# Kernel tuning notes

Measured on AMD Instinct MI355X. Metric: run time of the kernel, lower is better.

## Reference

```python
import jax, jax.numpy as jnp
import numpy as np
from jax import lax

B, T, D, K = 2, 4096, 128, 256


def setup_inputs() -> dict:
    key = jax.random.key(0)
    ks = jax.random.split(key, 5)
    s = 0.05
    return {
        "z": jax.random.normal(ks[0], (B, T, D), jnp.float32),
        "conv_kernel": jax.random.normal(ks[1], (K, 1, D), jnp.float32) * s,  # flax WIO depthwise
        "conv_bias": jnp.zeros((D,), jnp.float32),
        "Wq": jax.random.normal(ks[2], (D, D), jnp.float32) * s,
        "bq": jnp.zeros((D,), jnp.float32),
        "Wk": jax.random.normal(ks[3], (D, D), jnp.float32) * s,
        "bk": jnp.zeros((D,), jnp.float32),
        "Wo": jax.random.normal(ks[4], (D, D), jnp.float32) * s,
        "bo": jnp.zeros((D,), jnp.float32),
    }


def _sphere_norm(x):
    return x / jnp.maximum(jnp.linalg.norm(x, axis=-1, keepdims=True), 1e-8)


def reference(z, conv_kernel, conv_bias, Wq, bq, Wk, bk, Wo, bo):
    Bv, Tv, Dv = z.shape
    Kv = conv_kernel.shape[0]

    # Depthwise causal memory conv (flax nn.Conv, padding='CAUSAL', groups=D)
    memory_force = lax.conv_general_dilated(
        z, conv_kernel, window_strides=(1,), padding=[(Kv - 1, 0)],
        dimension_numbers=("NWC", "WIO", "NWC"), feature_group_count=Dv,
    ) + conv_bias

    # Keys are computed from the base point z once, shared across RK4 stages
    k_hat = _sphere_norm(z @ Wk + bk)  # [B,T,D]
    mask = jnp.tril(jnp.ones((Tv, Tv), z.dtype))  # causal mask

    def vector_field(z_curr):
        q_hat = _sphere_norm(z_curr @ Wq + bq)
        dots = jnp.einsum("btd,bsd->bts", q_hat, k_hat)  # [B,T,T]
        attn = jnp.sin(dots) * mask  # Kuramoto-style sin coupling, causal
        kuramoto = jnp.einsum("bts,bsd->btd", attn, k_hat) @ Wo + bo
        total = memory_force + kuramoto
        # project to tangent space of the sphere at z_curr
        return total - jnp.sum(total * z_curr, axis=-1, keepdims=True) * z_curr

    h = 1.0

    def retract(z_base, v):
        return _sphere_norm(z_base + v)

    k1 = vector_field(z)
    k2 = vector_field(retract(z, 0.5 * h * k1))
    k3 = vector_field(retract(z, 0.5 * h * k2))
    k4 = vector_field(retract(z, h * k3))
    v_final = (h / 6.0) * (k1 + 2 * k2 + 2 * k3 + k4)
    return retract(z, v_final)
```

## Files before the change

### kernel.cpp

```cpp
#include <hip/hip_runtime.h>
#include <hip/hip_bf16.h>

#define BB 2
#define TT 4096
#define DD 128
#define KK 256
#define NROW (BB*TT)
#define NELT (NROW*DD)

typedef _Float16 f16;
typedef __attribute__((ext_vector_type(8))) f16 half8;
typedef __attribute__((ext_vector_type(2))) __fp16 fp16x2;
typedef __attribute__((ext_vector_type(4))) float f32x4;
typedef __attribute__((ext_vector_type(2))) int i32x2;

__device__ __forceinline__ int pack2(float a, float b){
  fp16x2 h = __builtin_amdgcn_cvt_pkrtz(a, b);
  return __builtin_bit_cast(int, h);
}

__device__ __forceinline__ void stage_w_f16(int tid, const float* __restrict__ W, f16* Wh){
  #pragma unroll
  for (int it = 0; it < 8; it++){
    int idx = tid + it*256;
    f32x4 a = *(const f32x4*)(W + (size_t)idx*8);
    f32x4 b = *(const f32x4*)(W + (size_t)idx*8 + 4);
    half8 h;
    #pragma unroll
    for (int u = 0; u < 4; u++){ h[u] = (f16)a[u]; h[4+u] = (f16)b[u]; }
    *(half8*)(Wh + (size_t)idx*8) = h;
  }
}

__device__ __forceinline__ void proj_norm_rows(
    int tid, int r0,
    const float* __restrict__ src, const float* __restrict__ W, const float* __restrict__ bias,
    f16* __restrict__ dst, f16* __restrict__ dstT)
{
  __shared__ f16 Wh[DD*DD];
  __shared__ float zs[32*DD];
  stage_w_f16(tid, W, Wh);
  #pragma unroll
  for (int it = 0; it < 4; it++){
    int idx = tid + it*256;
    *(f32x4*)(zs + idx*4) = *(const f32x4*)(src + (size_t)r0*DD + idx*4);
  }
  __syncthreads();
  int c = tid & 15, rr = tid >> 4;
  float acc0[8], acc1[8];
  #pragma unroll
  for (int u = 0; u < 8; u++){ float bv = bias[c*8+u]; acc0[u] = bv; acc1[u] = bv; }
  const float* zr0 = zs + rr*DD;
  const float* zr1 = zs + (rr+16)*DD;
  #pragma unroll 4
  for (int i = 0; i < DD; i++){
    half8 wv = *(const half8*)(Wh + i*DD + c*8);
    float a0 = zr0[i], a1 = zr1[i];
    #pragma unroll
    for (int u = 0; u < 8; u++){
      float w = (float)wv[u];
      acc0[u] = fmaf(a0, w, acc0[u]);
      acc1[u] = fmaf(a1, w, acc1[u]);
    }
  }
  float s0 = 0.f, s1 = 0.f;
  #pragma unroll
  for (int u = 0; u < 8; u++){ s0 = fmaf(acc0[u], acc0[u], s0); s1 = fmaf(acc1[u], acc1[u], s1); }
  #pragma unroll
  for (int m = 1; m < 16; m <<= 1){ s0 += __shfl_xor(s0, m, 16); s1 += __shfl_xor(s1, m, 16); }
  float inv0 = 1.f / fmaxf(sqrtf(s0), 1e-8f);
  float inv1 = 1.f / fmaxf(sqrtf(s1), 1e-8f);
  half8 h0, h1;
  #pragma unroll
  for (int u = 0; u < 8; u++){ h0[u] = (f16)(acc0[u]*inv0); h1[u] = (f16)(acc1[u]*inv1); }
  int row0 = r0 + rr, row1 = row0 + 16;
  *(half8*)(dst + (size_t)row0*DD + c*8) = h0;
  *(half8*)(dst + (size_t)row1*DD + c*8) = h1;
  if (dstT){
    int b = row0 >> 12, t0 = row0 & 4095, t1 = row1 & 4095;
    #pragma unroll
    for (int u = 0; u < 8; u++){
      dstT[((size_t)b*DD + c*8 + u)*TT + t0] = h0[u];
      dstT[((size_t)b*DD + c*8 + u)*TT + t1] = h1[u];
    }
  }
}

__global__ __launch_bounds__(256) void k_prep(
    const float* __restrict__ z, const float* __restrict__ Wk, const float* __restrict__ bk,
    const float* __restrict__ ck, const float* __restrict__ cb,
    const float* __restrict__ Wq, const float* __restrict__ bq,
    f16* __restrict__ khb, f16* __restrict__ khT, f16* __restrict__ qhb,
    float* __restrict__ mf)
{
  int tid = threadIdx.x;
  if (blockIdx.x < 512){
    int bid = blockIdx.x;
    int d = tid & 127, tg = tid >> 7;
    int b = bid >> 8;
    int tbase = ((bid & 255) << 4) + tg*8;
    const float* zb = z + (size_t)b*TT*DD;
    float acc[8];
    #pragma unroll
    for (int j = 0; j < 8; j++) acc[j] = 0.f;
    float ckq[8];
    #pragma unroll
    for (int u = 0; u < 8; u++) ckq[u] = 0.f;
    int sstart = tbase - (KK-1);
    for (int ch = 0; ch < 33; ch++){
      #pragma unroll
      for (int u = 0; u < 8; u++){
        int base = ch*8 + u;
        int s = sstart + base;
        float zv = ((unsigned)s < (unsigned)TT && base < 263) ? zb[(size_t)s*DD + d] : 0.f;
        ckq[u] = (base < KK) ? ck[(size_t)base*DD + d] : 0.f;
        #pragma unroll
        for (int j = 0; j < 8; j++) acc[j] = fmaf(ckq[(u-j)&7], zv, acc[j]);
      }
    }
    float cbv = cb[d];
    #pragma unroll
    for (int j = 0; j < 8; j++)
      mf[((size_t)b*TT + tbase + j)*DD + d] = acc[j] + cbv;
  } else if (blockIdx.x < 768){
    proj_norm_rows(tid, (blockIdx.x - 512) * 32, z, Wk, bk, khb, khT);
  } else {
    proj_norm_rows(tid, (blockIdx.x - 768) * 32, z, Wq, bq, qhb, nullptr);
  }
}

#define QTILE 128
#define NQT3 (TT/QTILE)
#define NCHUNK 144

__global__ __launch_bounds__(256,2) void k_attn13(
    const f16* __restrict__ qhb, const f16* __restrict__ khb,
    const f16* __restrict__ khT, f16* __restrict__ part)
{
  int bid = blockIdx.x;
  int b = bid / NCHUNK;
  int rem = bid - b*NCHUNK;
  int qt = 0, chunk = 0;
  #pragma unroll 1
  for (int j = NQT3-1; j >= 0; j--){
    int nch = (j + 4) >> 2;
    if (rem < nch){ qt = j; chunk = rem; break; }
    rem -= nch;
  }
  int kt0 = chunk * 8;
  int kt1 = min(kt0 + 7, 2*qt + 1);
  int t0 = qt * QTILE;

  __shared__ __align__(16) f16 Kb[64*136];
  __shared__ __align__(16) f16 Kt[128*72];
  __shared__ __align__(16) f16 Ps[4][32*72];

  int tid  = threadIdx.x;
  int w    = tid >> 6;
  int lane = tid & 63;
  int n16  = lane & 15;
  int g    = lane >> 4;

  const f16* qg  = qhb + (size_t)b*TT*DD;
  const f16* kg  = khb + (size_t)b*TT*DD;
  const f16* ktg = khT + (size_t)b*DD*TT;

  int sb_r  = tid >> 4, sb_c = (tid & 15)*8;
  int st_r  = tid >> 3, st_c = (tid & 7)*8;

  half8 qa[2][4];
  #pragma unroll
  for (int p = 0; p < 2; p++){
    const f16* qrow = qg + (size_t)(t0 + 32*w + 16*p + n16)*DD + g*8;
    #pragma unroll
    for (int c = 0; c < 4; c++) qa[p][c] = *(const half8*)(qrow + 32*c);
  }
  f32x4 acc[2][8];
  #pragma unroll
  for (int p = 0; p < 2; p++)
    #pragma unroll
    for (int i = 0; i < 8; i++) acc[p][i] = (f32x4){0.f,0.f,0.f,0.f};

  f16* psw = &Ps[w][0];

  half8 sKb[4], sKt[4];
  {
    int s0 = kt0 * 64;
    #pragma unroll
    for (int it = 0; it < 4; it++)
      sKb[it] = *(const half8*)(kg + (size_t)(s0 + sb_r + it*16)*DD + sb_c);
    #pragma unroll
    for (int it = 0; it < 4; it++)
      sKt[it] = *(const half8*)(ktg + (size_t)(st_r + it*32)*TT + s0 + st_c);
  }

  for (int kt = kt0; kt <= kt1; kt++){
    #pragma unroll
    for (int it = 0; it < 4; it++)
      *(half8*)(Kb + (sb_r + it*16)*136 + sb_c) = sKb[it];
    #pragma unroll
    for (int it = 0; it < 4; it++)
      *(half8*)(Kt + (st_r + it*32)*72 + st_c) = sKt[it];
    __syncthreads();

    if (kt < kt1){
      int s0n = (kt+1) * 64;
      #pragma unroll
      for (int it = 0; it < 4; it++)
        sKb[it] = *(const half8*)(kg + (size_t)(s0n + sb_r + it*16)*DD + sb_c);
      #pragma unroll
      for (int it = 0; it < 4; it++)
        sKt[it] = *(const half8*)(ktg + (size_t)(st_r + it*32)*TT + s0n + st_c);
    }

    int s0 = kt * 64;
    f32x4 s_acc[2][4];
    #pragma unroll
    for (int p = 0; p < 2; p++)
      #pragma unroll
      for (int n = 0; n < 4; n++) s_acc[p][n] = (f32x4){0.f,0.f,0.f,0.f};
    #pragma unroll
    for (int c = 0; c < 4; c++){
      #pragma unroll
      for (int n = 0; n < 4; n++){
        half8 af = *(const half8*)(Kb + (16*n + n16)*136 + 32*c + g*8);
        s_acc[0][n] = __builtin_amdgcn_mfma_f32_16x16x32_f16(af, qa[0][c], s_acc[0][n], 0,0,0);
        s_acc[1][n] = __builtin_amdgcn_mfma_f32_16x16x32_f16(af, qa[1][c], s_acc[1][n], 0,0,0);
      }
    }
    #pragma unroll
    for (int p = 0; p < 2; p++){
      int qrow = t0 + 32*w + 16*p + n16;
      #pragma unroll
      for (int n = 0; n < 4; n++){
        int keyr = s0 + 16*n + 4*g;
        float v0 = (keyr     <= qrow) ? __sinf(s_acc[p][n][0]) : 0.f;
        float v1 = (keyr + 1 <= qrow) ? __sinf(s_acc[p][n][1]) : 0.f;
        float v2 = (keyr + 2 <= qrow) ? __sinf(s_acc[p][n][2]) : 0.f;
        float v3 = (keyr + 3 <= qrow) ? __sinf(s_acc[p][n][3]) : 0.f;
        i32x2 pw = { pack2(v0, v1), pack2(v2, v3) };
        *(i32x2*)(psw + (16*p + n16)*72 + 16*n + 4*g) = pw;
      }
    }

    #pragma unroll
    for (int h = 0; h < 2; h++){
      half8 pa[2];
      #pragma unroll
      for (int p = 0; p < 2; p++)
        pa[p] = *(const half8*)(psw + (16*p + n16)*72 + 32*h + 8*g);
      #pragma unroll
      for (int nt = 0; nt < 8; nt++){
        half8 bf = *(const half8*)(Kt + (16*nt + n16)*72 + 32*h + 8*g);
        acc[0][nt] = __builtin_amdgcn_mfma_f32_16x16x32_f16(pa[0], bf, acc[0][nt], 0,0,0);
        acc[1][nt] = __builtin_amdgcn_mfma_f32_16x16x32_f16(pa[1], bf, acc[1][nt], 0,0,0);
      }
    }
    __syncthreads();
  }

  f16* pb = part + (size_t)bid*(QTILE*DD) + (32*w)*DD;
  #pragma unroll
  for (int p = 0; p < 2; p++){
    #pragma unroll
    for (int nt = 0; nt < 8; nt++){
      #pragma unroll
      for (int r = 0; r < 4; r++){
        pb[(size_t)(16*p + 4*g + r)*DD + 16*nt + n16] = (f16)acc[p][nt][r];
      }
    }
  }
}

__global__ __launch_bounds__(256) void k_comb2(
    const float* __restrict__ z, const float* __restrict__ Wo, const float* __restrict__ bo,
    const float* __restrict__ mf, const f16* __restrict__ part,
    const float* __restrict__ zin, float* __restrict__ zout,
    float* __restrict__ vsum, float* __restrict__ out,
    const float* __restrict__ Wq, const float* __restrict__ bq, f16* __restrict__ qhb,
    float wsum, float cretr, int first, int last)
{
  __shared__ f16 Wh[DD*DD];
  __shared__ f16 Wqh[DD*DD];
  __shared__ float As[32*DD];
  int tid = threadIdx.x;
  int r0 = blockIdx.x * 32;
  stage_w_f16(tid, Wo, Wh);
  if (!last) stage_w_f16(tid, Wq, Wqh);
  {
    int b = r0 >> 12;
    int t = r0 & 4095;
    int qt = t >> 7;
    int ro = t & 127;
    int nc = (qt + 4) >> 2;
    int base = 0;
    #pragma unroll 1
    for (int j = NQT3-1; j > qt; j--) base += (j + 4) >> 2;
    size_t sb = ((size_t)b*NCHUNK + base)*(QTILE*DD) + (size_t)ro*DD;
    #pragma unroll
    for (int it = 0; it < 2; it++){
      int idx = tid + it*256;
      const f16* s = part + sb + (size_t)idx*8;
      float a[8];
      {
        half8 v = *(const half8*)(s);
        #pragma unroll
        for (int u = 0; u < 8; u++) a[u] = (float)v[u];
      }
      for (int cc = 1; cc < nc; cc++){
        half8 v = *(const half8*)(s + (size_t)cc*(QTILE*DD));
        #pragma unroll
        for (int u = 0; u < 8; u++) a[u] += (float)v[u];
      }
      f32x4 o0v = {a[0],a[1],a[2],a[3]}, o1v = {a[4],a[5],a[6],a[7]};
      *(f32x4*)(As + idx*8) = o0v;
      *(f32x4*)(As + idx*8 + 4) = o1v;
    }
  }
  __syncthreads();
  int c = tid & 15, rr = tid >> 4;
  float kur0[8], kur1[8];
  #pragma unroll
  for (int u = 0; u < 8; u++){ float bv = bo[c*8+u]; kur0[u] = bv; kur1[u] = bv; }
  const float* ar0 = As + rr*DD;
  const float* ar1 = As + (rr+16)*DD;
  #pragma unroll 4
  for (int i = 0; i < DD; i++){
    half8 wv = *(const half8*)(Wh + i*DD + c*8);
    float a0 = ar0[i], a1 = ar1[i];
    #pragma unroll
    for (int u = 0; u < 8; u++){
      float w = (float)wv[u];
      kur0[u] = fmaf(a0, w, kur0[u]);
      kur1[u] = fmaf(a1, w, kur1[u]);
    }
  }
  size_t o0 = (size_t)(r0+rr)*DD + c*8;
  size_t o1 = (size_t)(r0+rr+16)*DD + c*8;
  float tot0[8], tot1[8], zi0[8], zi1[8];
  {
    f32x4 m0a = *(const f32x4*)(mf + o0), m0b = *(const f32x4*)(mf + o0 + 4);
    f32x4 m1a = *(const f32x4*)(mf + o1), m1b = *(const f32x4*)(mf + o1 + 4);
    f32x4 z0a = *(const f32x4*)(zin + o0), z0b = *(const f32x4*)(zin + o0 + 4);
    f32x4 z1a = *(const f32x4*)(zin + o1), z1b = *(const f32x4*)(zin + o1 + 4);
    #pragma unroll
    for (int u = 0; u < 4; u++){
      tot0[u] = m0a[u] + kur0[u]; tot0[4+u] = m0b[u] + kur0[4+u];
      tot1[u] = m1a[u] + kur1[u]; tot1[4+u] = m1b[u] + kur1[4+u];
      zi0[u] = z0a[u]; zi0[4+u] = z0b[u];
      zi1[u] = z1a[u]; zi1[4+u] = z1b[u];
    }
  }
  float p0 = 0.f, p1 = 0.f;
  #pragma unroll
  for (int u = 0; u < 8; u++){ p0 = fmaf(tot0[u], zi0[u], p0); p1 = fmaf(tot1[u], zi1[u], p1); }
  #pragma unroll
  for (int m = 1; m < 16; m <<= 1){ p0 += __shfl_xor(p0, m, 16); p1 += __shfl_xor(p1, m, 16); }
  float ki0[8], ki1[8], vs0[8], vs1[8];
  #pragma unroll
  for (int u = 0; u < 8; u++){
    ki0[u] = tot0[u] - p0 * zi0[u];
    ki1[u] = tot1[u] - p1 * zi1[u];
  }
  if (first){
    #pragma unroll
    for (int u = 0; u < 8; u++){ vs0[u] = wsum*ki0[u]; vs1[u] = wsum*ki1[u]; }
  } else {
    f32x4 v0a = *(const f32x4*)(vsum + o0), v0b = *(const f32x4*)(vsum + o0 + 4);
    f32x4 v1a = *(const f32x4*)(vsum + o1), v1b = *(const f32x4*)(vsum + o1 + 4);
    #pragma unroll
    for (int u = 0; u < 4; u++){
      vs0[u] = fmaf(wsum, ki0[u], v0a[u]); vs0[4+u] = fmaf(wsum, ki0[4+u], v0b[u]);
      vs1[u] = fmaf(wsum, ki1[u], v1a[u]); vs1[4+u] = fmaf(wsum, ki1[4+u], v1b[u]);
    }
  }
  if (!last){
    f32x4 va = {vs0[0],vs0[1],vs0[2],vs0[3]}, vb = {vs0[4],vs0[5],vs0[6],vs0[7]};
    f32x4 vc = {vs1[0],vs1[1],vs1[2],vs1[3]}, vd = {vs1[4],vs1[5],vs1[6],vs1[7]};
    *(f32x4*)(vsum + o0) = va; *(f32x4*)(vsum + o0 + 4) = vb;
    *(f32x4*)(vsum + o1) = vc; *(f32x4*)(vsum + o1 + 4) = vd;
  }
  float nz0[8], nz1[8];
  {
    f32x4 z0a = *(const f32x4*)(z + o0), z0b = *(const f32x4*)(z + o0 + 4);
    f32x4 z1a = *(const f32x4*)(z + o1), z1b = *(const f32x4*)(z + o1 + 4);
    #pragma unroll
    for (int u = 0; u < 4; u++){
      float d0a = last ? vs0[u]*(1.f/6.f)   : cretr*ki0[u];
      float d0b = last ? vs0[4+u]*(1.f/6.f) : cretr*ki0[4+u];
      float d1a = last ? vs1[u]*(1.f/6.f)   : cretr*ki1[u];
      float d1b = last ? vs1[4+u]*(1.f/6.f) : cretr*ki1[4+u];
      nz0[u] = z0a[u] + d0a; nz0[4+u] = z0b[u] + d0b;
      nz1[u] = z1a[u] + d1a; nz1[4+u] = z1b[u] + d1b;
    }
  }
  float n0 = 0.f, n1 = 0.f;
  #pragma unroll
  for (int u = 0; u < 8; u++){ n0 = fmaf(nz0[u], nz0[u], n0); n1 = fmaf(nz1[u], nz1[u], n1); }
  #pragma unroll
  for (int m = 1; m < 16; m <<= 1){ n0 += __shfl_xor(n0, m, 16); n1 += __shfl_xor(n1, m, 16); }
  float i0 = 1.f / fmaxf(sqrtf(n0), 1e-8f);
  float i1 = 1.f / fmaxf(sqrtf(n1), 1e-8f);
  float* dst = last ? out : zout;
  f32x4 ra = {nz0[0]*i0, nz0[1]*i0, nz0[2]*i0, nz0[3]*i0};
  f32x4 rb = {nz0[4]*i0, nz0[5]*i0, nz0[6]*i0, nz0[7]*i0};
  f32x4 rc = {nz1[0]*i1, nz1[1]*i1, nz1[2]*i1, nz1[3]*i1};
  f32x4 rd = {nz1[4]*i1, nz1[5]*i1, nz1[6]*i1, nz1[7]*i1};
  *(f32x4*)(dst + o0) = ra; *(f32x4*)(dst + o0 + 4) = rb;
  *(f32x4*)(dst + o1) = rc; *(f32x4*)(dst + o1 + 4) = rd;

  if (!last){
    __syncthreads();
    *(f32x4*)(As + rr*DD + c*8)          = ra;
    *(f32x4*)(As + rr*DD + c*8 + 4)      = rb;
    *(f32x4*)(As + (rr+16)*DD + c*8)     = rc;
    *(f32x4*)(As + (rr+16)*DD + c*8 + 4) = rd;
    __syncthreads();
    float q0[8], q1[8];
    #pragma unroll
    for (int u = 0; u < 8; u++){ float bv = bq[c*8+u]; q0[u] = bv; q1[u] = bv; }
    const float* qr0 = As + rr*DD;
    const float* qr1 = As + (rr+16)*DD;
    #pragma unroll 4
    for (int i = 0; i < DD; i++){
      half8 wv = *(const half8*)(Wqh + i*DD + c*8);
      float a0 = qr0[i], a1 = qr1[i];
      #pragma unroll
      for (int u = 0; u < 8; u++){
        float w = (float)wv[u];
        q0[u] = fmaf(a0, w, q0[u]);
        q1[u] = fmaf(a1, w, q1[u]);
      }
    }
    float s0 = 0.f, s1 = 0.f;
    #pragma unroll
    for (int u = 0; u < 8; u++){ s0 = fmaf(q0[u], q0[u], s0); s1 = fmaf(q1[u], q1[u], s1); }
    #pragma unroll
    for (int m = 1; m < 16; m <<= 1){ s0 += __shfl_xor(s0, m, 16); s1 += __shfl_xor(s1, m, 16); }
    float qi0 = 1.f / fmaxf(sqrtf(s0), 1e-8f);
    float qi1 = 1.f / fmaxf(sqrtf(s1), 1e-8f);
    half8 h0, h1;
    #pragma unroll
    for (int u = 0; u < 8; u++){ h0[u] = (f16)(q0[u]*qi0); h1[u] = (f16)(q1[u]*qi1); }
    *(half8*)(qhb + (size_t)(r0+rr)*DD + c*8)    = h0;
    *(half8*)(qhb + (size_t)(r0+rr+16)*DD + c*8) = h1;
  }
}

extern "C" void kernel_launch(void* const* d_in, const int* in_sizes, int n_in,
                              void* d_out, int out_size, void* d_ws, size_t ws_size,
                              hipStream_t stream) {
  const float* z  = (const float*)d_in[0];
  const float* ck = (const float*)d_in[1];
  const float* cb = (const float*)d_in[2];
  const float* Wq = (const float*)d_in[3];
  const float* bq = (const float*)d_in[4];
  const float* Wk = (const float*)d_in[5];
  const float* bk = (const float*)d_in[6];
  const float* Wo = (const float*)d_in[7];
  const float* bo = (const float*)d_in[8];
  float* out = (float*)d_out;

  float* mf   = (float*)d_ws;
  float* zc   = mf   + NELT;
  float* vsum = zc   + NELT;
  f16*   khb  = (f16*)(vsum + NELT);
  f16*   khT  = khb  + NELT;
  f16*   qhb  = khT  + NELT;
  f16*   part = qhb  + NELT;

  k_prep<<<1024, 256, 0, stream>>>(z, Wk, bk, ck, cb, Wq, bq, khb, khT, qhb, mf);

  const float wv[4] = {1.f, 2.f, 2.f, 1.f};
  const float cv[4] = {0.5f, 0.5f, 1.f, 0.f};
  for (int st = 0; st < 4; st++){
    const float* zcur = (st == 0) ? z : zc;
    k_attn13<<<BB*NCHUNK, 256, 0, stream>>>(qhb, khb, khT, part);
    k_comb2 <<<NROW/32, 256, 0, stream>>>(z, Wo, bo, mf, part, zcur, zc, vsum, out,
                                          Wq, bq, qhb, wv[st], cv[st], st == 0, st == 3);
  }
}
```

Baseline: 285.6 us.

## Split attention tile across 8 waves with 16 query rows each

The attention kernel now launches 512 threads per block (8 waves), each wave owning 16 query rows instead of 32. This halves per-thread accumulator and prefetch registers and spreads the shared K-tile staging over more threads. The goal is more latency hiding and higher occupancy. In exchange, each wave reloads the K fragments from LDS for fewer MFMAs, and block-level syncs cover twice as many waves.

```diff
diff --git a/kernel.cpp b/kernel.cpp
--- a/kernel.cpp
+++ b/kernel.cpp
@@ -133,7 +133,7 @@
 #define NQT3 (TT/QTILE)
 #define NCHUNK 144
 
-__global__ __launch_bounds__(256,2) void k_attn13(
+__global__ __launch_bounds__(512,4) void k_attn15(
     const f16* __restrict__ qhb, const f16* __restrict__ khb,
     const f16* __restrict__ khT, f16* __restrict__ part)
 {
@@ -153,7 +153,7 @@
 
   __shared__ __align__(16) f16 Kb[64*136];
   __shared__ __align__(16) f16 Kt[128*72];
-  __shared__ __align__(16) f16 Ps[4][32*72];
+  __shared__ __align__(16) f16 Ps[8][16*72];
 
   int tid  = threadIdx.x;
   int w    = tid >> 6;
@@ -168,106 +168,92 @@
   int sb_r  = tid >> 4, sb_c = (tid & 15)*8;
   int st_r  = tid >> 3, st_c = (tid & 7)*8;
 
-  half8 qa[2][4];
-  #pragma unroll
-  for (int p = 0; p < 2; p++){
-    const f16* qrow = qg + (size_t)(t0 + 32*w + 16*p + n16)*DD + g*8;
-    #pragma unroll
-    for (int c = 0; c < 4; c++) qa[p][c] = *(const half8*)(qrow + 32*c);
-  }
-  f32x4 acc[2][8];
-  #pragma unroll
-  for (int p = 0; p < 2; p++)
-    #pragma unroll
-    for (int i = 0; i < 8; i++) acc[p][i] = (f32x4){0.f,0.f,0.f,0.f};
+  half8 qa[4];
+  {
+    const f16* qrow = qg + (size_t)(t0 + 16*w + n16)*DD + g*8;
+    #pragma unroll
+    for (int c = 0; c < 4; c++) qa[c] = *(const half8*)(qrow + 32*c);
+  }
+  f32x4 acc[8];
+  #pragma unroll
+  for (int i = 0; i < 8; i++) acc[i] = (f32x4){0.f,0.f,0.f,0.f};
 
   f16* psw = &Ps[w][0];
 
-  half8 sKb[4], sKt[4];
+  half8 sKb[2], sKt[2];
   {
     int s0 = kt0 * 64;
     #pragma unroll
-    for (int it = 0; it < 4; it++)
-      sKb[it] = *(const half8*)(kg + (size_t)(s0 + sb_r + it*16)*DD + sb_c);
-    #pragma unroll
-    for (int it = 0; it < 4; it++)
-      sKt[it] = *(const half8*)(ktg + (size_t)(st_r + it*32)*TT + s0 + st_c);
+    for (int it = 0; it < 2; it++)
+      sKb[it] = *(const half8*)(kg + (size_t)(s0 + sb_r + it*32)*DD + sb_c);
+    #pragma unroll
+    for (int it = 0; it < 2; it++)
+      sKt[it] = *(const half8*)(ktg + (size_t)(st_r + it*64)*TT + s0 + st_c);
   }
 
   for (int kt = kt0; kt <= kt1; kt++){
     #pragma unroll
-    for (int it = 0; it < 4; it++)
-      *(half8*)(Kb + (sb_r + it*16)*136 + sb_c) = sKb[it];
-    #pragma unroll
-    for (int it = 0; it < 4; it++)
-      *(half8*)(Kt + (st_r + it*32)*72 + st_c) = sKt[it];
+    for (int it = 0; it < 2; it++)
+      *(half8*)(Kb + (sb_r + it*32)*136 + sb_c) = sKb[it];
+    #pragma unroll
+    for (int it = 0; it < 2; it++)
+      *(half8*)(Kt + (st_r + it*64)*72 + st_c) = sKt[it];
     __syncthreads();
 
     if (kt < kt1){
       int s0n = (kt+1) * 64;
       #pragma unroll
-      for (int it = 0; it < 4; it++)
-        sKb[it] = *(const half8*)(kg + (size_t)(s0n + sb_r + it*16)*DD + sb_c);
-      #pragma unroll
-      for (int it = 0; it < 4; it++)
-        sKt[it] = *(const half8*)(ktg + (size_t)(st_r + it*32)*TT + s0n + st_c);
+      for (int it = 0; it < 2; it++)
+        sKb[it] = *(const half8*)(kg + (size_t)(s0n + sb_r + it*32)*DD + sb_c);
+      #pragma unroll
+      for (int it = 0; it < 2; it++)
+        sKt[it] = *(const half8*)(ktg + (size_t)(st_r + it*64)*TT + s0n + st_c);
     }
 
     int s0 = kt * 64;
-    f32x4 s_acc[2][4];
-    #pragma unroll
-    for (int p = 0; p < 2; p++)
-      #pragma unroll
-      for (int n = 0; n < 4; n++) s_acc[p][n] = (f32x4){0.f,0.f,0.f,0.f};
+    f32x4 s_acc[4];
+    #pragma unroll
+    for (int n = 0; n < 4; n++) s_acc[n] = (f32x4){0.f,0.f,0.f,0.f};
     #pragma unroll
     for (int c = 0; c < 4; c++){
       #pragma unroll
       for (int n = 0; n < 4; n++){
         half8 af = *(const half8*)(Kb + (16*n + n16)*136 + 32*c + g*8);
-        s_acc[0][n] = __builtin_amdgcn_mfma_f32_16x16x32_f16(af, qa[0][c], s_acc[0][n], 0,0,0);
-        s_acc[1][n] = __builtin_amdgcn_mfma_f32_16x16x32_f16(af, qa[1][c], s_acc[1][n], 0,0,0);
-      }
-    }
-    #pragma unroll
-    for (int p = 0; p < 2; p++){
-      int qrow = t0 + 32*w + 16*p + n16;
+        s_acc[n] = __builtin_amdgcn_mfma_f32_16x16x32_f16(af, qa[c], s_acc[n], 0,0,0);
+      }
+    }
+    {
+      int qrow = t0 + 16*w + n16;
       #pragma unroll
       for (int n = 0; n < 4; n++){
         int keyr = s0 + 16*n + 4*g;
-        float v0 = (keyr     <= qrow) ? __sinf(s_acc[p][n][0]) : 0.f;
-        float v1 = (keyr + 1 <= qrow) ? __sinf(s_acc[p][n][1]) : 0.f;
-        float v2 = (keyr + 2 <= qrow) ? __sinf(s_acc[p][n][2]) : 0.f;
-        float v3 = (keyr + 3 <= qrow) ? __sinf(s_acc[p][n][3]) : 0.f;
+        float v0 = (keyr     <= qrow) ? __sinf(s_acc[n][0]) : 0.f;
+        float v1 = (keyr + 1 <= qrow) ? __sinf(s_acc[n][1]) : 0.f;
+        float v2 = (keyr + 2 <= qrow) ? __sinf(s_acc[n][2]) : 0.f;
+        float v3 = (keyr + 3 <= qrow) ? __sinf(s_acc[n][3]) : 0.f;
         i32x2 pw = { pack2(v0, v1), pack2(v2, v3) };
-        *(i32x2*)(psw + (16*p + n16)*72 + 16*n + 4*g) = pw;
+        *(i32x2*)(psw + n16*72 + 16*n + 4*g) = pw;
       }
     }
 
     #pragma unroll
     for (int h = 0; h < 2; h++){
-      half8 pa[2];
-      #pragma unroll
-      for (int p = 0; p < 2; p++)
-        pa[p] = *(const half8*)(psw + (16*p + n16)*72 + 32*h + 8*g);
+      half8 pa = *(const half8*)(psw + n16*72 + 32*h + 8*g);
       #pragma unroll
       for (int nt = 0; nt < 8; nt++){
         half8 bf = *(const half8*)(Kt + (16*nt + n16)*72 + 32*h + 8*g);
-        acc[0][nt] = __builtin_amdgcn_mfma_f32_16x16x32_f16(pa[0], bf, acc[0][nt], 0,0,0);
-        acc[1][nt] = __builtin_amdgcn_mfma_f32_16x16x32_f16(pa[1], bf, acc[1][nt], 0,0,0);
+        acc[nt] = __builtin_amdgcn_mfma_f32_16x16x32_f16(pa, bf, acc[nt], 0,0,0);
       }
     }
     __syncthreads();
   }
 
-  f16* pb = part + (size_t)bid*(QTILE*DD) + (32*w)*DD;
-  #pragma unroll
-  for (int p = 0; p < 2; p++){
-    #pragma unroll
-    for (int nt = 0; nt < 8; nt++){
-      #pragma unroll
-      for (int r = 0; r < 4; r++){
-        pb[(size_t)(16*p + 4*g + r)*DD + 16*nt + n16] = (f16)acc[p][nt][r];
-      }
+  f16* pb = part + (size_t)bid*(QTILE*DD) + (size_t)(16*w)*DD;
+  #pragma unroll
+  for (int nt = 0; nt < 8; nt++){
+    #pragma unroll
+    for (int r = 0; r < 4; r++){
+      pb[(size_t)(4*g + r)*DD + 16*nt + n16] = (f16)acc[nt][r];
     }
   }
 }
@@ -475,7 +461,7 @@
   const float cv[4] = {0.5f, 0.5f, 1.f, 0.f};
   for (int st = 0; st < 4; st++){
     const float* zcur = (st == 0) ? z : zc;
-    k_attn13<<<BB*NCHUNK, 256, 0, stream>>>(qhb, khb, khT, part);
+    k_attn15<<<BB*NCHUNK, 512, 0, stream>>>(qhb, khb, khT, part);
     k_comb2 <<<NROW/32, 256, 0, stream>>>(z, Wo, bo, mf, part, zcur, zc, vsum, out,
                                           Wq, bq, qhb, wv[st], cv[st], st == 0, st == 3);
   }
```

After: 296.0 us. 3.6% more time.

## Switch attention kernel to 32x32 MFMA with register-resident P and double-buffered K

Applied to the files above, without the earlier changes.

Rewrites the attention kernel to use 32x32x16 MFMA tiles instead of 16x16x32. The sin-scores P are rearranged in registers with cross-half-wave shuffles rather than round-tripped through shared memory. The K tiles are double-buffered so there is one barrier per iteration instead of two. The intent is to cut LDS traffic and synchronization, at the cost of higher register pressure from the f32x16 accumulators and more shared memory.

```diff
diff --git a/kernel.cpp b/kernel.cpp
--- a/kernel.cpp
+++ b/kernel.cpp
@@ -12,7 +12,9 @@
 typedef __attribute__((ext_vector_type(8))) f16 half8;
 typedef __attribute__((ext_vector_type(2))) __fp16 fp16x2;
 typedef __attribute__((ext_vector_type(4))) float f32x4;
+typedef __attribute__((ext_vector_type(16))) float f32x16;
 typedef __attribute__((ext_vector_type(2))) int i32x2;
+typedef __attribute__((ext_vector_type(4))) int i32x4;
 
 __device__ __forceinline__ int pack2(float a, float b){
   fp16x2 h = __builtin_amdgcn_cvt_pkrtz(a, b);
@@ -133,7 +135,7 @@
 #define NQT3 (TT/QTILE)
 #define NCHUNK 144
 
-__global__ __launch_bounds__(256,2) void k_attn13(
+__global__ __launch_bounds__(256,2) void k_attn17(
     const f16* __restrict__ qhb, const f16* __restrict__ khb,
     const f16* __restrict__ khT, f16* __restrict__ part)
 {
@@ -151,15 +153,14 @@
   int kt1 = min(kt0 + 7, 2*qt + 1);
   int t0 = qt * QTILE;
 
-  __shared__ __align__(16) f16 Kb[64*136];
-  __shared__ __align__(16) f16 Kt[128*72];
-  __shared__ __align__(16) f16 Ps[4][32*72];
+  __shared__ __align__(16) f16 KbD[2][64*136];
+  __shared__ __align__(16) f16 KtD[2][128*72];
 
   int tid  = threadIdx.x;
   int w    = tid >> 6;
   int lane = tid & 63;
-  int n16  = lane & 15;
-  int g    = lane >> 4;
+  int q31  = lane & 31;
+  int hi   = lane >> 5;
 
   const f16* qg  = qhb + (size_t)b*TT*DD;
   const f16* kg  = khb + (size_t)b*TT*DD;
@@ -168,20 +169,20 @@
   int sb_r  = tid >> 4, sb_c = (tid & 15)*8;
   int st_r  = tid >> 3, st_c = (tid & 7)*8;
 
-  half8 qa[2][4];
-  #pragma unroll
-  for (int p = 0; p < 2; p++){
-    const f16* qrow = qg + (size_t)(t0 + 32*w + 16*p + n16)*DD + g*8;
-    #pragma unroll
-    for (int c = 0; c < 4; c++) qa[p][c] = *(const half8*)(qrow + 32*c);
-  }
-  f32x4 acc[2][8];
-  #pragma unroll
-  for (int p = 0; p < 2; p++)
-    #pragma unroll
-    for (int i = 0; i < 8; i++) acc[p][i] = (f32x4){0.f,0.f,0.f,0.f};
-
-  f16* psw = &Ps[w][0];
+  int qrow_g = t0 + 32*w + q31;
+
+  half8 qb[8];
+  {
+    const f16* qrow = qg + (size_t)qrow_g*DD + 8*hi;
+    #pragma unroll
+    for (int ks = 0; ks < 8; ks++) qb[ks] = *(const half8*)(qrow + 16*ks);
+  }
+
+  f32x16 acc[4];
+  #pragma unroll
+  for (int d = 0; d < 4; d++)
+    #pragma unroll
+    for (int i = 0; i < 16; i++) acc[d][i] = 0.f;
 
   half8 sKb[4], sKt[4];
   {
@@ -192,16 +193,20 @@
     #pragma unroll
     for (int it = 0; it < 4; it++)
       sKt[it] = *(const half8*)(ktg + (size_t)(st_r + it*32)*TT + s0 + st_c);
-  }
-
+    #pragma unroll
+    for (int it = 0; it < 4; it++)
+      *(half8*)(&KbD[0][0] + (sb_r + it*16)*136 + sb_c) = sKb[it];
+    #pragma unroll
+    for (int it = 0; it < 4; it++)
+      *(half8*)(&KtD[0][0] + (st_r + it*32)*72 + st_c) = sKt[it];
+  }
+  __syncthreads();
+
+  #pragma unroll 1
   for (int kt = kt0; kt <= kt1; kt++){
-    #pragma unroll
-    for (int it = 0; it < 4; it++)
-      *(half8*)(Kb + (sb_r + it*16)*136 + sb_c) = sKb[it];
-    #pragma unroll
-    for (int it = 0; it < 4; it++)
-      *(half8*)(Kt + (st_r + it*32)*72 + st_c) = sKt[it];
-    __syncthreads();
+    int cur = (kt - kt0) & 1;
+    const f16* KbL = &KbD[cur][0];
+    const f16* KtL = &KtD[cur][0];
 
     if (kt < kt1){
       int s0n = (kt+1) * 64;
@@ -214,60 +219,77 @@
     }
 
     int s0 = kt * 64;
-    f32x4 s_acc[2][4];
-    #pragma unroll
-    for (int p = 0; p < 2; p++)
-      #pragma unroll
-      for (int n = 0; n < 4; n++) s_acc[p][n] = (f32x4){0.f,0.f,0.f,0.f};
-    #pragma unroll
-    for (int c = 0; c < 4; c++){
-      #pragma unroll
-      for (int n = 0; n < 4; n++){
-        half8 af = *(const half8*)(Kb + (16*n + n16)*136 + 32*c + g*8);
-        s_acc[0][n] = __builtin_amdgcn_mfma_f32_16x16x32_f16(af, qa[0][c], s_acc[0][n], 0,0,0);
-        s_acc[1][n] = __builtin_amdgcn_mfma_f32_16x16x32_f16(af, qa[1][c], s_acc[1][n], 0,0,0);
+    f32x16 sa0, sa1;
+    #pragma unroll
+    for (int i = 0; i < 16; i++){ sa0[i] = 0.f; sa1[i] = 0.f; }
+    #pragma unroll
+    for (int ks = 0; ks < 8; ks++){
+      half8 a0 = *(const half8*)(KbL + (q31)      *136 + 16*ks + 8*hi);
+      half8 a1 = *(const half8*)(KbL + (32 + q31) *136 + 16*ks + 8*hi);
+      sa0 = __builtin_amdgcn_mfma_f32_32x32x16_f16(a0, qb[ks], sa0, 0,0,0);
+      sa1 = __builtin_amdgcn_mfma_f32_32x32x16_f16(a1, qb[ks], sa1, 0,0,0);
+    }
+
+    float p0v[16], p1v[16];
+    #pragma unroll
+    for (int r = 0; r < 16; r++){
+      int kr = (r&3) + 8*(r>>2) + 4*hi;
+      p0v[r] = (s0 + kr      <= qrow_g) ? __sinf(sa0[r]) : 0.f;
+      p1v[r] = (s0 + 32 + kr <= qrow_g) ? __sinf(sa1[r]) : 0.f;
+    }
+
+    half8 pf[4];
+    #pragma unroll
+    for (int kb = 0; kb < 2; kb++){
+      const float* pv = kb ? p1v : p0v;
+      #pragma unroll
+      for (int u = 0; u < 2; u++){
+        int pl0 = pack2(pv[8*u+0], pv[8*u+1]);
+        int pl1 = pack2(pv[8*u+2], pv[8*u+3]);
+        int ph0 = pack2(pv[8*u+4], pv[8*u+5]);
+        int ph1 = pack2(pv[8*u+6], pv[8*u+7]);
+        int xl0 = __shfl_xor(pl0, 32);
+        int xl1 = __shfl_xor(pl1, 32);
+        int xh0 = __shfl_xor(ph0, 32);
+        int xh1 = __shfl_xor(ph1, 32);
+        i32x4 fr;
+        fr[0] = hi ? xh0 : pl0;
+        fr[1] = hi ? xh1 : pl1;
+        fr[2] = hi ? ph0 : xl0;
+        fr[3] = hi ? ph1 : xl1;
+        pf[2*kb+u] = __builtin_bit_cast(half8, fr);
       }
     }
-    #pragma unroll
-    for (int p = 0; p < 2; p++){
-      int qrow = t0 + 32*w + 16*p + n16;
-      #pragma unroll
-      for (int n = 0; n < 4; n++){
-        int keyr = s0 + 16*n + 4*g;
-        float v0 = (keyr     <= qrow) ? __sinf(s_acc[p][n][0]) : 0.f;
-        float v1 = (keyr + 1 <= qrow) ? __sinf(s_acc[p][n][1]) : 0.f;
-        float v2 = (keyr + 2 <= qrow) ? __sinf(s_acc[p][n][2]) : 0.f;
-        float v3 = (keyr + 3 <= qrow) ? __sinf(s_acc[p][n][3]) : 0.f;
-        i32x2 pw = { pack2(v0, v1), pack2(v2, v3) };
-        *(i32x2*)(psw + (16*p + n16)*72 + 16*n + 4*g) = pw;
+
+    #pragma unroll
+    for (int s = 0; s < 4; s++){
+      #pragma unroll
+      for (int d0 = 0; d0 < 4; d0++){
+        half8 bf = *(const half8*)(KtL + (32*d0 + q31)*72 + 16*s + 8*hi);
+        acc[d0] = __builtin_amdgcn_mfma_f32_32x32x16_f16(pf[s], bf, acc[d0], 0,0,0);
       }
     }
 
-    #pragma unroll
-    for (int h = 0; h < 2; h++){
-      half8 pa[2];
-      #pragma unroll
-      for (int p = 0; p < 2; p++)
-        pa[p] = *(const half8*)(psw + (16*p + n16)*72 + 32*h + 8*g);
-      #pragma unroll
-      for (int nt = 0; nt < 8; nt++){
-        half8 bf = *(const half8*)(Kt + (16*nt + n16)*72 + 32*h + 8*g);
-        acc[0][nt] = __builtin_amdgcn_mfma_f32_16x16x32_f16(pa[0], bf, acc[0][nt], 0,0,0);
-        acc[1][nt] = __builtin_amdgcn_mfma_f32_16x16x32_f16(pa[1], bf, acc[1][nt], 0,0,0);
-      }
-    }
-    __syncthreads();
-  }
-
-  f16* pb = part + (size_t)bid*(QTILE*DD) + (32*w)*DD;
-  #pragma unroll
-  for (int p = 0; p < 2; p++){
-    #pragma unroll
-    for (int nt = 0; nt < 8; nt++){
-      #pragma unroll
-      for (int r = 0; r < 4; r++){
-        pb[(size_t)(16*p + 4*g + r)*DD + 16*nt + n16] = (f16)acc[p][nt][r];
-      }
+    if (kt < kt1){
+      f16* KbN = &KbD[cur^1][0];
+      f16* KtN = &KtD[cur^1][0];
+      #pragma unroll
+      for (int it = 0; it < 4; it++)
+        *(half8*)(KbN + (sb_r + it*16)*136 + sb_c) = sKb[it];
+      #pragma unroll
+      for (int it = 0; it < 4; it++)
+        *(half8*)(KtN + (st_r + it*32)*72 + st_c) = sKt[it];
+      __syncthreads();
+    }
+  }
+
+  f16* pb = part + (size_t)bid*(QTILE*DD);
+  #pragma unroll
+  for (int d0 = 0; d0 < 4; d0++){
+    #pragma unroll
+    for (int r = 0; r < 16; r++){
+      int qr = 32*w + (r&3) + 8*(r>>2) + 4*hi;
+      pb[(size_t)qr*DD + 32*d0 + q31] = (f16)acc[d0][r];
     }
   }
 }
@@ -475,7 +497,7 @@
   const float cv[4] = {0.5f, 0.5f, 1.f, 0.f};
   for (int st = 0; st < 4; st++){
     const float* zcur = (st == 0) ? z : zc;
-    k_attn13<<<BB*NCHUNK, 256, 0, stream>>>(qhb, khb, khT, part);
+    k_attn17<<<BB*NCHUNK, 256, 0, stream>>>(qhb, khb, khT, part);
     k_comb2 <<<NROW/32, 256, 0, stream>>>(z, Wo, bo, mf, part, zcur, zc, vsum, out,
                                           Wq, bq, qhb, wv[st], cv[st], st == 0, st == 3);
   }
```

New measurement: 275.2 us. -3.7%, faster.
